# Optimization experiments

Measured on AMD Instinct MI355X. Metric: run time of the kernel, lower is better.

Reference implementation:

```python
import jax, jax.numpy as jnp
import numpy as np

N = 100000      # nodes
NNZ = 1600000   # edges (avg degree 16)
F_IN = 128
F_OUT = 128


def setup_inputs() -> dict:
    key = jax.random.key(0)
    ks = jax.random.split(key, 8)
    return {
        "features": jax.random.normal(ks[0], (N, F_IN), dtype=jnp.float32),
        "edge_val": jax.random.uniform(ks[1], (NNZ,), dtype=jnp.float32),
        "W1": jax.random.normal(ks[2], (F_IN, F_OUT), dtype=jnp.float32) * 0.05,
        "b1": jax.random.normal(ks[3], (F_OUT,), dtype=jnp.float32) * 0.05,
        "W2": jax.random.normal(ks[4], (F_IN, F_OUT), dtype=jnp.float32) * 0.05,
        "b2": jax.random.normal(ks[5], (F_OUT,), dtype=jnp.float32) * 0.05,
        "edge_row": jax.random.randint(ks[6], (NNZ,), 0, N, dtype=jnp.int32),
        "edge_col": jax.random.randint(ks[7], (NNZ,), 0, N, dtype=jnp.int32),
    }


def _spmm(edge_val, edge_row, edge_col, x, n):
    # sparse (n,n) COO matrix @ dense (n,f): gather cols, scale, scatter-add rows
    gathered = edge_val[:, None] * x[edge_col]          # (nnz, f)
    return jax.ops.segment_sum(gathered, edge_row, num_segments=n)


def reference(features, edge_val, W1, b1, W2, b2, edge_row, edge_col):
    n = features.shape[0]
    Lf = _spmm(edge_val, edge_row, edge_col, features, n)   # L2 @ features
    inter_feature = Lf * features                            # elementwise mul
    # L1 = L + I, so L1 @ features == Lf + features (selfLoop is identity)
    inter_part1 = (Lf + features) @ W1 + b1                  # self.linear
    Li = _spmm(edge_val, edge_row, edge_col, inter_feature, n)
    inter_part2 = Li @ W2 + b2                               # interActTransform
    return inter_part1 + inter_part2
```

## Files before the change

### kernel.cpp

```cpp
#include <hip/hip_runtime.h>

#define F 128
#define NBSHIFT 7
#define CAPB 3072
#define CHUNK 8192
#define NBMAX 1024

typedef __attribute__((ext_vector_type(8))) short bf16x8;
typedef __attribute__((ext_vector_type(4))) float f32x4;

__device__ inline float bf2f(unsigned short u) {
    union { unsigned int i; float f; } x;
    x.i = ((unsigned int)u) << 16;
    return x.f;
}
__device__ inline unsigned short f2bf(float f) {
    union { float f; unsigned int i; } x;
    x.f = f;
    unsigned int lsb = (x.i >> 16) & 1;
    x.i += 0x7FFFu + lsb;
    return (unsigned short)(x.i >> 16);
}

__global__ __launch_bounds__(256) void prep(
    const float* __restrict__ feat, unsigned short* __restrict__ feat_h, int total4,
    const float* __restrict__ W1, const float* __restrict__ W2,
    unsigned short* __restrict__ Wp,
    const int* __restrict__ er, const int* __restrict__ ec,
    const float* __restrict__ ev,
    int* __restrict__ gcnt, uint2* __restrict__ gbuf, int nnz, int nb, int nbin)
{
    __shared__ int hist[NBMAX];
    __shared__ int base[NBMAX];
    const int bid = blockIdx.x;
    const int tid = threadIdx.x;

    if (bid < nbin) {
        const int e0 = bid * CHUNK;
        int rreg[32];

        for (int b = tid; b < nb; b += 256) hist[b] = 0;
        __syncthreads();

#pragma unroll
        for (int k = 0; k < 32; ++k) {
            int e = e0 + k * 256 + tid;
            int r = (e < nnz) ? er[e] : -1;
            rreg[k] = r;
            if (r >= 0) atomicAdd(&hist[r >> NBSHIFT], 1);
        }
        __syncthreads();

        for (int b = tid; b < nb; b += 256) {
            int h = hist[b];
            base[b] = h ? atomicAdd(&gcnt[b], h) : 0;
            hist[b] = 0;
        }
        __syncthreads();

#pragma unroll
        for (int k = 0; k < 32; ++k) {
            int r = rreg[k];
            if (r >= 0) {
                int e = e0 + k * 256 + tid;
                int b = r >> NBSHIFT;
                int rank = atomicAdd(&hist[b], 1);
                int idx  = base[b] + rank;
                if (idx >= CAPB) idx = CAPB - 1;
                unsigned int q = (unsigned int)__float2int_rn(ev[e] * 32767.f);
                gbuf[(size_t)b * CAPB + idx] =
                    make_uint2((q << 17) | (unsigned int)ec[e], (unsigned int)r);
            }
        }
    } else if (bid < nbin + 16) {
        int idx = (bid - nbin) * 256 + tid;
        if (idx < 8 * 8 * 64) {
            int lane = idx & 63;
            int ks   = (idx >> 6) & 7;
            int nt   = idx >> 9;
            int col  = nt * 16 + (lane & 15);
            int krow = ks * 32 + (lane >> 4) * 8;
            const float* W = (krow < 128) ? (W1 + (size_t)krow * F)
                                          : (W2 + (size_t)(krow - 128) * F);
            unsigned short o[8];
#pragma unroll
            for (int j = 0; j < 8; ++j) o[j] = f2bf(W[(size_t)j * F + col]);
            unsigned short* dst = Wp + (size_t)idx * 8;
            *(ushort4*)(dst)     = make_ushort4(o[0], o[1], o[2], o[3]);
            *(ushort4*)(dst + 4) = make_ushort4(o[4], o[5], o[6], o[7]);
        }
    } else {
        int i = (bid - nbin - 16) * 256 + tid;
        if (i < total4) {
            float4 v = *(const float4*)(feat + (size_t)i * 4);
            ushort4 o;
            o.x = f2bf(v.x); o.y = f2bf(v.y); o.z = f2bf(v.z); o.w = f2bf(v.w);
            *(ushort4*)(feat_h + (size_t)i * 4) = o;
        }
    }
}

__global__ __launch_bounds__(256) void bucket_to_rows(
    const int* __restrict__ gcnt, const uint2* __restrict__ gbuf,
    int* __restrict__ cnt, unsigned int* __restrict__ recs, int n, int cap)
{
    __shared__ unsigned int slots[128][68];
    __shared__ int lcnt[128];
    const int b = blockIdx.x;
    const int tid = threadIdx.x;
    const int base_row = b << NBSHIFT;

    for (int r = tid; r < 128; r += 256) lcnt[r] = 0;
    __syncthreads();

    int nrec = gcnt[b];
    if (nrec > CAPB) nrec = CAPB;
    const uint2* gb = gbuf + (size_t)b * CAPB;
    for (int i = tid; i < nrec; i += 256) {
        uint2 rec = gb[i];
        int r = (int)rec.y - base_row;
        int pos = atomicAdd(&lcnt[r], 1);
        if (pos < cap) slots[r][pos] = rec.x;
    }
    __syncthreads();

    const int sub = tid & 3;
    for (int rr = tid >> 2; rr < 128; rr += 64) {
        int row = base_row + rr;
        if (row >= n) continue;
        int c = lcnt[rr];
        if (c > cap) c = cap;
        if (sub == 0) cnt[row] = c;
        uint4* dst = (uint4*)(recs + (size_t)row * cap);
        for (int q = sub; q * 4 < c; q += 4)
            dst[q] = *(const uint4*)&slots[rr][q * 4];
    }
}

__device__ inline float4 row_gather(
    const unsigned short* __restrict__ src,
    const unsigned int* __restrict__ rp, int e, int f)
{
    float4 A0 = {0.f,0.f,0.f,0.f}, A1 = {0.f,0.f,0.f,0.f};
    float4 A2 = {0.f,0.f,0.f,0.f}, A3 = {0.f,0.f,0.f,0.f};
    int i = 0;
    for (; i + 7 < e; i += 8) {
        uint4 ua = *(const uint4*)(rp + i);
        uint4 ub = *(const uint4*)(rp + i + 4);
        ushort4 x0 = *(const ushort4*)(src + (size_t)(ua.x & 0x1FFFF) * F + f);
        ushort4 x1 = *(const ushort4*)(src + (size_t)(ua.y & 0x1FFFF) * F + f);
        ushort4 x2 = *(const ushort4*)(src + (size_t)(ua.z & 0x1FFFF) * F + f);
        ushort4 x3 = *(const ushort4*)(src + (size_t)(ua.w & 0x1FFFF) * F + f);
        ushort4 x4 = *(const ushort4*)(src + (size_t)(ub.x & 0x1FFFF) * F + f);
        ushort4 x5 = *(const ushort4*)(src + (size_t)(ub.y & 0x1FFFF) * F + f);
        ushort4 x6 = *(const ushort4*)(src + (size_t)(ub.z & 0x1FFFF) * F + f);
        ushort4 x7 = *(const ushort4*)(src + (size_t)(ub.w & 0x1FFFF) * F + f);
        float v0 = (float)(ua.x >> 17) * (1.f / 32767.f);
        float v1 = (float)(ua.y >> 17) * (1.f / 32767.f);
        float v2 = (float)(ua.z >> 17) * (1.f / 32767.f);
        float v3 = (float)(ua.w >> 17) * (1.f / 32767.f);
        float v4 = (float)(ub.x >> 17) * (1.f / 32767.f);
        float v5 = (float)(ub.y >> 17) * (1.f / 32767.f);
        float v6 = (float)(ub.z >> 17) * (1.f / 32767.f);
        float v7 = (float)(ub.w >> 17) * (1.f / 32767.f);
        A0.x += v0 * bf2f(x0.x); A0.y += v0 * bf2f(x0.y);
        A0.z += v0 * bf2f(x0.z); A0.w += v0 * bf2f(x0.w);
        A1.x += v1 * bf2f(x1.x); A1.y += v1 * bf2f(x1.y);
        A1.z += v1 * bf2f(x1.z); A1.w += v1 * bf2f(x1.w);
        A2.x += v2 * bf2f(x2.x); A2.y += v2 * bf2f(x2.y);
        A2.z += v2 * bf2f(x2.z); A2.w += v2 * bf2f(x2.w);
        A3.x += v3 * bf2f(x3.x); A3.y += v3 * bf2f(x3.y);
        A3.z += v3 * bf2f(x3.z); A3.w += v3 * bf2f(x3.w);
        A0.x += v4 * bf2f(x4.x); A0.y += v4 * bf2f(x4.y);
        A0.z += v4 * bf2f(x4.z); A0.w += v4 * bf2f(x4.w);
        A1.x += v5 * bf2f(x5.x); A1.y += v5 * bf2f(x5.y);
        A1.z += v5 * bf2f(x5.z); A1.w += v5 * bf2f(x5.w);
        A2.x += v6 * bf2f(x6.x); A2.y += v6 * bf2f(x6.y);
        A2.z += v6 * bf2f(x6.z); A2.w += v6 * bf2f(x6.w);
        A3.x += v7 * bf2f(x7.x); A3.y += v7 * bf2f(x7.y);
        A3.z += v7 * bf2f(x7.z); A3.w += v7 * bf2f(x7.w);
    }
    for (; i + 3 < e; i += 4) {
        uint4 ua = *(const uint4*)(rp + i);
        ushort4 x0 = *(const ushort4*)(src + (size_t)(ua.x & 0x1FFFF) * F + f);
        ushort4 x1 = *(const ushort4*)(src + (size_t)(ua.y & 0x1FFFF) * F + f);
        ushort4 x2 = *(const ushort4*)(src + (size_t)(ua.z & 0x1FFFF) * F + f);
        ushort4 x3 = *(const ushort4*)(src + (size_t)(ua.w & 0x1FFFF) * F + f);
        float v0 = (float)(ua.x >> 17) * (1.f / 32767.f);
        float v1 = (float)(ua.y >> 17) * (1.f / 32767.f);
        float v2 = (float)(ua.z >> 17) * (1.f / 32767.f);
        float v3 = (float)(ua.w >> 17) * (1.f / 32767.f);
        A0.x += v0 * bf2f(x0.x); A0.y += v0 * bf2f(x0.y);
        A0.z += v0 * bf2f(x0.z); A0.w += v0 * bf2f(x0.w);
        A1.x += v1 * bf2f(x1.x); A1.y += v1 * bf2f(x1.y);
        A1.z += v1 * bf2f(x1.z); A1.w += v1 * bf2f(x1.w);
        A2.x += v2 * bf2f(x2.x); A2.y += v2 * bf2f(x2.y);
        A2.z += v2 * bf2f(x2.z); A2.w += v2 * bf2f(x2.w);
        A3.x += v3 * bf2f(x3.x); A3.y += v3 * bf2f(x3.y);
        A3.z += v3 * bf2f(x3.z); A3.w += v3 * bf2f(x3.w);
    }
    for (; i < e; ++i) {
        unsigned int u0 = rp[i];
        float v0 = (float)(u0 >> 17) * (1.f / 32767.f);
        ushort4 x0 = *(const ushort4*)(src + (size_t)(u0 & 0x1FFFF) * F + f);
        A0.x += v0 * bf2f(x0.x); A0.y += v0 * bf2f(x0.y);
        A0.z += v0 * bf2f(x0.z); A0.w += v0 * bf2f(x0.w);
    }
    float4 acc;
    acc.x = (A0.x + A1.x) + (A2.x + A3.x);
    acc.y = (A0.y + A1.y) + (A2.y + A3.y);
    acc.z = (A0.z + A1.z) + (A2.z + A3.z);
    acc.w = (A0.w + A1.w) + (A2.w + A3.w);
    return acc;
}

__global__ __launch_bounds__(256) void spmm_feat(
    const unsigned short* __restrict__ feat_h, const float* __restrict__ feat,
    const int* __restrict__ cnt, const unsigned int* __restrict__ recs,
    unsigned short* __restrict__ A1_h, unsigned short* __restrict__ P_h,
    int n, int cap)
{
    int gid = blockIdx.x * 256 + threadIdx.x;
    int row = gid >> 5;
    if (row >= n) return;
    int f = (gid & 31) << 2;
    int e = cnt[row];
    if (e > cap) e = cap;
    float4 acc = row_gather(feat_h, recs + (size_t)row * cap, e, f);

    size_t o = (size_t)row * F + f;
    float4 ft = *(const float4*)(feat + o);

    ushort4 a1;
    a1.x = f2bf(acc.x + ft.x);
    a1.y = f2bf(acc.y + ft.y);
    a1.z = f2bf(acc.z + ft.z);
    a1.w = f2bf(acc.w + ft.w);
    *(ushort4*)(A1_h + o) = a1;

    ushort4 ph;
    ph.x = f2bf(acc.x * ft.x);
    ph.y = f2bf(acc.y * ft.y);
    ph.z = f2bf(acc.z * ft.z);
    ph.w = f2bf(acc.w * ft.w);
    *(ushort4*)(P_h + o) = ph;
}

__global__ __launch_bounds__(256) void spmm_inter(
    const unsigned short* __restrict__ P_h,
    const int* __restrict__ cnt, const unsigned int* __restrict__ recs,
    unsigned short* __restrict__ Li_h, int n, int cap)
{
    int gid = blockIdx.x * 256 + threadIdx.x;
    int row = gid >> 5;
    if (row >= n) return;
    int f = (gid & 31) << 2;
    int e = cnt[row];
    if (e > cap) e = cap;
    float4 acc = row_gather(P_h, recs + (size_t)row * cap, e, f);

    ushort4 lh;
    lh.x = f2bf(acc.x);
    lh.y = f2bf(acc.y);
    lh.z = f2bf(acc.z);
    lh.w = f2bf(acc.w);
    *(ushort4*)(Li_h + (size_t)row * F + f) = lh;
}

__global__ __launch_bounds__(256) void gemm_mfma(
    const unsigned short* __restrict__ A1_h,
    const unsigned short* __restrict__ Li_h,
    const unsigned short* __restrict__ Wp,
    const float* __restrict__ b1, const float* __restrict__ b2,
    float* __restrict__ out, int n)
{
    const int wave = threadIdx.x >> 6;
    const int lane = threadIdx.x & 63;
    const int quad = lane >> 4;
    const int l16  = lane & 15;
    const int row0 = blockIdx.x * 64 + wave * 16;

    int arow = row0 + l16;
    if (arow >= n) arow = n - 1;

    f32x4 acc[8];
#pragma unroll
    for (int t = 0; t < 8; ++t) acc[t] = (f32x4){0.f, 0.f, 0.f, 0.f};

    const unsigned short* A1p = A1_h + (size_t)arow * F + quad * 8;
    const unsigned short* A2p = Li_h + (size_t)arow * F + quad * 8;

#pragma unroll
    for (int ks = 0; ks < 8; ++ks) {
        const unsigned short* ap = (ks < 4) ? (A1p + ks * 32) : (A2p + (ks - 4) * 32);
        bf16x8 a = *(const bf16x8*)ap;
#pragma unroll
        for (int t = 0; t < 8; ++t) {
            bf16x8 b = *(const bf16x8*)(Wp + ((size_t)(t * 8 + ks) * 64 + lane) * 8);
            acc[t] = __builtin_amdgcn_mfma_f32_16x16x32_bf16(a, b, acc[t], 0, 0, 0);
        }
    }

    const int orow0 = row0 + quad * 4;
#pragma unroll
    for (int t = 0; t < 8; ++t) {
        int col = t * 16 + l16;
        float bias = b1[col] + b2[col];
#pragma unroll
        for (int r = 0; r < 4; ++r) {
            int gr = orow0 + r;
            if (gr < n) out[(size_t)gr * F + col] = acc[t][r] + bias;
        }
    }
}

extern "C" void kernel_launch(void* const* d_in, const int* in_sizes, int n_in,
                              void* d_out, int out_size, void* d_ws, size_t ws_size,
                              hipStream_t stream)
{
    const float* feat = (const float*)d_in[0];
    const float* ev   = (const float*)d_in[1];
    const float* W1   = (const float*)d_in[2];
    const float* b1   = (const float*)d_in[3];
    const float* W2   = (const float*)d_in[4];
    const float* b2   = (const float*)d_in[5];
    const int*   er   = (const int*)d_in[6];
    const int*   ec   = (const int*)d_in[7];

    const int n   = in_sizes[0] / F;
    const int nnz = in_sizes[1];
    int nb = (n + 127) >> NBSHIFT;
    if (nb > NBMAX) nb = NBMAX;

    char* ws = (char*)d_ws;
    unsigned short* feat_h = (unsigned short*)ws;  ws += (size_t)n * F * sizeof(short);
    unsigned short* A1_h   = (unsigned short*)ws;  ws += (size_t)n * F * sizeof(short);
    unsigned short* P_h    = (unsigned short*)ws;  ws += (size_t)n * F * sizeof(short);
    unsigned short* Li_h   = (unsigned short*)ws;  ws += (size_t)n * F * sizeof(short);
    unsigned short* Wp     = (unsigned short*)ws;  ws += (size_t)8 * 8 * 64 * 8 * sizeof(short);
    int* cnt               = (int*)ws;             ws += (size_t)n * sizeof(int);
    int* gcnt              = (int*)ws;             ws += (size_t)nb * sizeof(int);
    unsigned int* recs     = (unsigned int*)ws;

    uint2* gbuf = (uint2*)Li_h;

    size_t used  = (size_t)(ws - (char*)d_ws);
    size_t avail = (ws_size > used) ? (ws_size - used) : 0;
    int cap = (int)(avail / ((size_t)n * sizeof(unsigned int)));
    if (cap > 64) cap = 64;
    cap &= ~3;

    hipMemsetAsync(gcnt, 0, (size_t)nb * sizeof(int), stream);

    const int total4 = n * F / 4;
    const int nbin = (nnz + CHUNK - 1) / CHUNK;
    const int conv_blocks = (total4 + 255) / 256;
    prep<<<nbin + 16 + conv_blocks, 256, 0, stream>>>(
        feat, feat_h, total4, W1, W2, Wp, er, ec, ev, gcnt, gbuf, nnz, nb, nbin);

    bucket_to_rows<<<nb, 256, 0, stream>>>(gcnt, gbuf, cnt, recs, n, cap);

    int spmm_blocks = (n * 32 + 255) / 256;
    spmm_feat<<<spmm_blocks, 256, 0, stream>>>(feat_h, feat, cnt, recs,
                                               A1_h, P_h, n, cap);
    spmm_inter<<<spmm_blocks, 256, 0, stream>>>(P_h, cnt, recs, Li_h, n, cap);

    gemm_mfma<<<(n + 63) / 64, 256, 0, stream>>>(A1_h, Li_h, Wp, b1, b2,
                                                 (float*)d_out, n);
}
```

Measured before the change: 346.5 us.

## Fuse second SpMM into MFMA GEMM via shared-memory tile; read bf16 self features

Merges the second sparse gather (Li = L @ P) into the GEMM kernel. Each block gathers 64 rows into a padded LDS tile and feeds it directly to the MFMA loop, so the Li intermediate no longer makes a round trip through global memory and one launch is dropped. The feature SpMM now reads the self features from the bf16 copy instead of fp32, which halves that read but adds rounding error to A1 and P. The fused kernel has fewer blocks, each doing serial gathers over 8 rows per thread before the GEMM, which could reduce latency hiding.

```diff
diff --git a/kernel.cpp b/kernel.cpp
--- a/kernel.cpp
+++ b/kernel.cpp
@@ -5,16 +5,17 @@
 #define CAPB 3072
 #define CHUNK 8192
 #define NBMAX 1024
+#define LIPITCH 144
 
 typedef __attribute__((ext_vector_type(8))) short bf16x8;
 typedef __attribute__((ext_vector_type(4))) float f32x4;
 
-__device__ inline float bf2f(unsigned short u) {
+__device__ __forceinline__ float bf2f(unsigned short u) {
     union { unsigned int i; float f; } x;
     x.i = ((unsigned int)u) << 16;
     return x.f;
 }
-__device__ inline unsigned short f2bf(float f) {
+__device__ __forceinline__ unsigned short f2bf(float f) {
     union { float f; unsigned int i; } x;
     x.f = f;
     unsigned int lsb = (x.i >> 16) & 1;
@@ -137,7 +138,7 @@
     }
 }
 
-__device__ inline float4 row_gather(
+__device__ __forceinline__ float4 row_gather(
     const unsigned short* __restrict__ src,
     const unsigned int* __restrict__ rp, int e, int f)
 {
@@ -215,7 +216,7 @@
 }
 
 __global__ __launch_bounds__(256) void spmm_feat(
-    const unsigned short* __restrict__ feat_h, const float* __restrict__ feat,
+    const unsigned short* __restrict__ feat_h,
     const int* __restrict__ cnt, const unsigned int* __restrict__ recs,
     unsigned short* __restrict__ A1_h, unsigned short* __restrict__ P_h,
     int n, int cap)
@@ -229,7 +230,9 @@
     float4 acc = row_gather(feat_h, recs + (size_t)row * cap, e, f);
 
     size_t o = (size_t)row * F + f;
-    float4 ft = *(const float4*)(feat + o);
+    ushort4 fh = *(const ushort4*)(feat_h + o);
+    float4 ft;
+    ft.x = bf2f(fh.x); ft.y = bf2f(fh.y); ft.z = bf2f(fh.z); ft.w = bf2f(fh.w);
 
     ushort4 a1;
     a1.x = f2bf(acc.x + ft.x);
@@ -246,36 +249,37 @@
     *(ushort4*)(P_h + o) = ph;
 }
 
-__global__ __launch_bounds__(256) void spmm_inter(
+__global__ __launch_bounds__(256) void spmm2_gemm(
     const unsigned short* __restrict__ P_h,
-    const int* __restrict__ cnt, const unsigned int* __restrict__ recs,
-    unsigned short* __restrict__ Li_h, int n, int cap)
-{
-    int gid = blockIdx.x * 256 + threadIdx.x;
-    int row = gid >> 5;
-    if (row >= n) return;
-    int f = (gid & 31) << 2;
-    int e = cnt[row];
-    if (e > cap) e = cap;
-    float4 acc = row_gather(P_h, recs + (size_t)row * cap, e, f);
-
-    ushort4 lh;
-    lh.x = f2bf(acc.x);
-    lh.y = f2bf(acc.y);
-    lh.z = f2bf(acc.z);
-    lh.w = f2bf(acc.w);
-    *(ushort4*)(Li_h + (size_t)row * F + f) = lh;
-}
-
-__global__ __launch_bounds__(256) void gemm_mfma(
     const unsigned short* __restrict__ A1_h,
-    const unsigned short* __restrict__ Li_h,
     const unsigned short* __restrict__ Wp,
     const float* __restrict__ b1, const float* __restrict__ b2,
-    float* __restrict__ out, int n)
-{
-    const int wave = threadIdx.x >> 6;
-    const int lane = threadIdx.x & 63;
+    const int* __restrict__ cnt, const unsigned int* __restrict__ recs,
+    float* __restrict__ out, int n, int cap)
+{
+    __shared__ unsigned short li[64][LIPITCH];
+    const int tid  = threadIdx.x;
+    const int fs   = (tid & 31) << 2;
+    const int rsub = tid >> 5;
+
+#pragma unroll
+    for (int k = 0; k < 8; ++k) {
+        int rl  = rsub + k * 8;
+        int row = blockIdx.x * 64 + rl;
+        ushort4 lh = make_ushort4(0, 0, 0, 0);
+        if (row < n) {
+            int e = cnt[row];
+            if (e > cap) e = cap;
+            float4 acc = row_gather(P_h, recs + (size_t)row * cap, e, fs);
+            lh.x = f2bf(acc.x); lh.y = f2bf(acc.y);
+            lh.z = f2bf(acc.z); lh.w = f2bf(acc.w);
+        }
+        *(ushort4*)&li[rl][fs] = lh;
+    }
+    __syncthreads();
+
+    const int wave = tid >> 6;
+    const int lane = tid & 63;
     const int quad = lane >> 4;
     const int l16  = lane & 15;
     const int row0 = blockIdx.x * 64 + wave * 16;
@@ -288,12 +292,12 @@
     for (int t = 0; t < 8; ++t) acc[t] = (f32x4){0.f, 0.f, 0.f, 0.f};
 
     const unsigned short* A1p = A1_h + (size_t)arow * F + quad * 8;
-    const unsigned short* A2p = Li_h + (size_t)arow * F + quad * 8;
+    const unsigned short* lp  = &li[wave * 16 + l16][quad * 8];
 
 #pragma unroll
     for (int ks = 0; ks < 8; ++ks) {
-        const unsigned short* ap = (ks < 4) ? (A1p + ks * 32) : (A2p + (ks - 4) * 32);
-        bf16x8 a = *(const bf16x8*)ap;
+        bf16x8 a = (ks < 4) ? *(const bf16x8*)(A1p + ks * 32)
+                            : *(const bf16x8*)(lp + (ks - 4) * 32);
 #pragma unroll
         for (int t = 0; t < 8; ++t) {
             bf16x8 b = *(const bf16x8*)(Wp + ((size_t)(t * 8 + ks) * 64 + lane) * 8);
@@ -336,13 +340,12 @@
     unsigned short* feat_h = (unsigned short*)ws;  ws += (size_t)n * F * sizeof(short);
     unsigned short* A1_h   = (unsigned short*)ws;  ws += (size_t)n * F * sizeof(short);
     unsigned short* P_h    = (unsigned short*)ws;  ws += (size_t)n * F * sizeof(short);
-    unsigned short* Li_h   = (unsigned short*)ws;  ws += (size_t)n * F * sizeof(short);
     unsigned short* Wp     = (unsigned short*)ws;  ws += (size_t)8 * 8 * 64 * 8 * sizeof(short);
     int* cnt               = (int*)ws;             ws += (size_t)n * sizeof(int);
     int* gcnt              = (int*)ws;             ws += (size_t)nb * sizeof(int);
     unsigned int* recs     = (unsigned int*)ws;
 
-    uint2* gbuf = (uint2*)Li_h;
+    uint2* gbuf = (uint2*)A1_h;
 
     size_t used  = (size_t)(ws - (char*)d_ws);
     size_t avail = (ws_size > used) ? (ws_size - used) : 0;
@@ -361,10 +364,9 @@
     bucket_to_rows<<<nb, 256, 0, stream>>>(gcnt, gbuf, cnt, recs, n, cap);
 
     int spmm_blocks = (n * 32 + 255) / 256;
-    spmm_feat<<<spmm_blocks, 256, 0, stream>>>(feat_h, feat, cnt, recs,
+    spmm_feat<<<spmm_blocks, 256, 0, stream>>>(feat_h, cnt, recs,
                                                A1_h, P_h, n, cap);
-    spmm_inter<<<spmm_blocks, 256, 0, stream>>>(P_h, cnt, recs, Li_h, n, cap);
-
-    gemm_mfma<<<(n + 63) / 64, 256, 0, stream>>>(A1_h, Li_h, Wp, b1, b2,
-                                                 (float*)d_out, n);
-}
+
+    spmm2_gemm<<<(n + 63) / 64, 256, 0, stream>>>(P_h, A1_h, Wp, b1, b2,
+                                                  cnt, recs, (float*)d_out, n, cap);
+}
```

After: 339.1 us. 2.1% less time.
